# Optimization experiments

Measured on AMD Instinct MI355X. Metric: run time of the kernel, lower is better.

Reference implementation:

```python
import jax, jax.numpy as jnp
import numpy as np

B, L, ENC_IN, DM, H, HD, DFF, NL, C_OUT = 4, 1024, 64, 512, 8, 64, 2048, 3, 64
SCALE = 1.0 / np.sqrt(HD)


def _ln(x, g, b):
    m = x.mean(-1, keepdims=True)
    v = ((x - m) ** 2).mean(-1, keepdims=True)
    return (x - m) / jnp.sqrt(v + 1e-5) * g + b


def _pos_encoding(length, d):
    pos = np.arange(length)[:, None].astype(np.float32)
    div = np.exp(np.arange(0, d, 2).astype(np.float32) * (-np.log(10000.0) / d))
    pe = np.zeros((length, d), np.float32)
    pe[:, 0::2] = np.sin(pos * div)
    pe[:, 1::2] = np.cos(pos * div)
    return jnp.asarray(pe)

PE = _pos_encoding(L, DM)


def _prob_attn(q, k, v, idx):
    # q,k,v: [B,H,L,D]; idx: [L, sample_k] random key indices per query
    qk = jnp.einsum('bhqd,bhkd->bhqk', q, k)                       # [B,H,L,L]
    qks = jnp.take_along_axis(qk, idx[None, None, :, :], axis=-1)   # sampled QK
    M = qks.max(-1) - qks.sum(-1) / L                                # sparsity measure [B,H,L]
    _, top = jax.lax.top_k(M, L)  # n_top == L here (degenerate full selection / permutation)
    scores = jnp.take_along_axis(qk, top[..., None], axis=2) * SCALE  # gathered Q rows
    A = jax.nn.softmax(scores, axis=-1)
    return jnp.einsum('bhuk,bhkd->bhud', A, v)                       # [B,H,L,D]


def _forward(x_enc, sample_idx, W_emb, b_emb, Wq, bq, Wk, bk, Wv, bv, Wo, bo,
             W1, b1, W2, b2, g1, be1, g2, be2, gN, bN, W_proj, b_proj):
    x = x_enc @ W_emb + b_emb + PE[None]  # [B,L,DM]
    for i in range(NL):
        q = (x @ Wq[i] + bq[i]).reshape(B, L, H, HD).transpose(0, 2, 1, 3)
        k = (x @ Wk[i] + bk[i]).reshape(B, L, H, HD).transpose(0, 2, 1, 3)
        v = (x @ Wv[i] + bv[i]).reshape(B, L, H, HD).transpose(0, 2, 1, 3)
        o = _prob_attn(q, k, v, sample_idx[i]).transpose(0, 2, 1, 3).reshape(B, L, DM)
        o = o @ Wo[i] + bo[i]
        x = _ln(x + o, g1[i], be1[i])
        y = jax.nn.gelu(x @ W1[i] + b1[i], approximate=False) @ W2[i] + b2[i]
        x = _ln(x + y, g2[i], be2[i])
    x = _ln(x, gN, bN)
    return x @ W_proj + b_proj


def setup_inputs() -> dict:
    key = jax.random.key(0)
    ks = jax.random.split(key, 16)
    nrm = lambda k, s: jax.random.normal(k, s, jnp.float32) * 0.02
    return {
        'x_enc': jax.random.normal(ks[0], (B, L, ENC_IN), jnp.float32),
        'sample_idx': jax.random.randint(ks[1], (NL, L, L), 0, L, dtype=jnp.int32),
        'W_emb': nrm(ks[2], (ENC_IN, DM)), 'b_emb': jnp.zeros((DM,), jnp.float32),
        'Wq': nrm(ks[3], (NL, DM, DM)), 'bq': jnp.zeros((NL, DM), jnp.float32),
        'Wk': nrm(ks[4], (NL, DM, DM)), 'bk': jnp.zeros((NL, DM), jnp.float32),
        'Wv': nrm(ks[5], (NL, DM, DM)), 'bv': jnp.zeros((NL, DM), jnp.float32),
        'Wo': nrm(ks[6], (NL, DM, DM)), 'bo': jnp.zeros((NL, DM), jnp.float32),
        'W1': nrm(ks[7], (NL, DM, DFF)), 'b1': jnp.zeros((NL, DFF), jnp.float32),
        'W2': nrm(ks[8], (NL, DFF, DM)), 'b2': jnp.zeros((NL, DM), jnp.float32),
        'g1': jnp.ones((NL, DM), jnp.float32), 'be1': jnp.zeros((NL, DM), jnp.float32),
        'g2': jnp.ones((NL, DM), jnp.float32), 'be2': jnp.zeros((NL, DM), jnp.float32),
        'gN': jnp.ones((DM,), jnp.float32), 'bN': jnp.zeros((DM,), jnp.float32),
        'W_proj': nrm(ks[9], (DM, C_OUT)), 'b_proj': jnp.zeros((C_OUT,), jnp.float32),
    }


def reference(x_enc, sample_idx, W_emb, b_emb, Wq, bq, Wk, bk, Wv, bv, Wo, bo,
              W1, b1, W2, b2, g1, be1, g2, be2, gN, bN, W_proj, b_proj):
    return _forward(x_enc, sample_idx, W_emb, b_emb, Wq, bq, Wk, bk, Wv, bv, Wo, bo,
                    W1, b1, W2, b2, g1, be1, g2, be2, gN, bN, W_proj, b_proj)
```

## Files before the change

### kernel.cpp

```cpp
#include <hip/hip_runtime.h>
#include <cstdint>
#include <cstddef>

#define B_    4
#define L_    1024
#define ENCIN 64
#define DM    512
#define H_    8
#define HD    64
#define DFF   2048
#define NL    3
#define COUT  64
#define SCALE 0.125f
#define BH    32

typedef __attribute__((ext_vector_type(4))) short short4v;
typedef __attribute__((ext_vector_type(8))) short short8v;
typedef __attribute__((ext_vector_type(4))) float f32x4;
typedef unsigned short u16;

#define MFMA16(a,b,c) __builtin_amdgcn_mfma_f32_16x16x32_bf16(a,b,c,0,0,0)

#define GL2LDS(gsrc, ldst) \
  __builtin_amdgcn_global_load_lds( \
      (const __attribute__((address_space(1))) void*)(uintptr_t)(const void*)(gsrc), \
      (__attribute__((address_space(3))) void*)(uintptr_t)(const void*)(ldst), 16, 0, 0)

__device__ __forceinline__ u16 f2bf(float f){
  unsigned u = __float_as_uint(f);
  u += 0x7fffu + ((u >> 16) & 1u);
  return (u16)(u >> 16);
}
__device__ __forceinline__ float bf2f(u16 h){
  return __uint_as_float(((unsigned)h) << 16);
}
__device__ __forceinline__ void split2(float v, u16* h, u16* l){
  u16 hh = f2bf(v);
  *h = hh;
  *l = f2bf(v - bf2f(hh));
}

template<int BN, int MODE>
__global__ __launch_bounds__(256) void hgemm(
    const u16* __restrict__ Ah, const u16* __restrict__ Al,
    const u16* __restrict__ Bh, const u16* __restrict__ Bl,
    const float* __restrict__ bias,
    float* __restrict__ o32, u16* __restrict__ oh, u16* __restrict__ ol,
    int M, int N, int K)
{
  constexpr int NT = BN / 32;
  __shared__ u16 As0[128*32], As1[128*32];
  __shared__ u16 Bs0[BN*32],  Bs1[BN*32];
  const int t = threadIdx.x, lane = t & 63, wid = t >> 6;
  const int wr = wid >> 1, wc = wid & 1;
  const int fr = lane & 15, fq = lane >> 4;
  const int m0 = blockIdx.y * 128, n0 = blockIdx.x * BN;
  const int arow = lane >> 2, aseg = lane & 3;

  f32x4 acc[4][NT] = {};

  for (int kt = 0; kt < K; kt += 32) {
#pragma unroll
    for (int i = 0; i < 2; i++) {
      int c = wid + 4*i;
      GL2LDS(&Ah[(size_t)(m0 + c*16 + arow)*K + kt + aseg*8], &As0[c*512]);
      GL2LDS(&Al[(size_t)(m0 + c*16 + arow)*K + kt + aseg*8], &As1[c*512]);
    }
#pragma unroll
    for (int i = 0; i < BN/64; i++) {
      int c = wid + 4*i;
      GL2LDS(&Bh[(size_t)(n0 + c*16 + arow)*K + kt + aseg*8], &Bs0[c*512]);
      GL2LDS(&Bl[(size_t)(n0 + c*16 + arow)*K + kt + aseg*8], &Bs1[c*512]);
    }
    __syncthreads();

    short8v a0[4], a1[4], b0[NT], b1[NT];
#pragma unroll
    for (int m = 0; m < 4; m++) {
      int off = (wr*64 + m*16 + fr)*32 + fq*4;
      short4v x0 = *(const short4v*)&As0[off];
      short4v x1 = *(const short4v*)&As0[off + 16];
      a0[m] = __builtin_shufflevector(x0, x1, 0,1,2,3,4,5,6,7);
      short4v y0 = *(const short4v*)&As1[off];
      short4v y1 = *(const short4v*)&As1[off + 16];
      a1[m] = __builtin_shufflevector(y0, y1, 0,1,2,3,4,5,6,7);
    }
#pragma unroll
    for (int n = 0; n < NT; n++) {
      int off = (wc*(BN/2) + n*16 + fr)*32 + fq*4;
      short4v x0 = *(const short4v*)&Bs0[off];
      short4v x1 = *(const short4v*)&Bs0[off + 16];
      b0[n] = __builtin_shufflevector(x0, x1, 0,1,2,3,4,5,6,7);
      short4v y0 = *(const short4v*)&Bs1[off];
      short4v y1 = *(const short4v*)&Bs1[off + 16];
      b1[n] = __builtin_shufflevector(y0, y1, 0,1,2,3,4,5,6,7);
    }
#pragma unroll
    for (int m = 0; m < 4; m++)
#pragma unroll
      for (int n = 0; n < NT; n++) {
        acc[m][n] = MFMA16(a0[m], b0[n], acc[m][n]);
        acc[m][n] = MFMA16(a0[m], b1[n], acc[m][n]);
        acc[m][n] = MFMA16(a1[m], b0[n], acc[m][n]);
      }
    __syncthreads();
  }

#pragma unroll
  for (int m = 0; m < 4; m++) {
    int gr0 = m0 + wr*64 + m*16 + fq*4;
#pragma unroll
    for (int n = 0; n < NT; n++) {
      int gc = n0 + wc*(BN/2) + n*16 + fr;
      float bv = bias[gc];
#pragma unroll
      for (int r = 0; r < 4; r++) {
        float v = acc[m][n][r] + bv;
        int row = gr0 + r;
        if (MODE == 0) {
          o32[(size_t)row*N + gc] = v;
        } else if (MODE == 1) {
          int li = row & (L_ - 1);
          float dv = expf((float)(gc & ~1) * -0.017988946039015984f);
          float ang = (float)li * dv;
          v += (gc & 1) ? cosf(ang) : sinf(ang);
          size_t ix = (size_t)row*N + gc;
          o32[ix] = v;
          split2(v, &oh[ix], &ol[ix]);
        } else if (MODE == 2) {
          float gv = 0.5f * v * (1.0f + erff(v * 0.70710678118654752f));
          size_t ix = (size_t)row*N + gc;
          split2(gv, &oh[ix], &ol[ix]);
        } else if (MODE == 3) {
          int b = row >> 10, li = row & (L_ - 1);
          int hh2 = gc >> 6, d = gc & 63;
          size_t ix = (((size_t)(b*H_ + hh2))*L_ + li)*HD + d;
          split2(v, &oh[ix], &ol[ix]);
        } else if (MODE == 4) {
          int b = row >> 10, li = row & (L_ - 1);
          int hh2 = gc >> 6, d = gc & 63;
          size_t ix = (((size_t)(b*H_ + hh2))*HD + d)*L_ + li;
          oh[ix] = f2bf(v);
        }
      }
    }
  }
}

__global__ __launch_bounds__(256) void qk_mfma(
    const u16* __restrict__ qh, const u16* __restrict__ ql,
    const u16* __restrict__ kh, const u16* __restrict__ kl,
    float* __restrict__ S)
{
  __shared__ u16 Qs0[128*64], Qs1[128*64], Ks0[128*64], Ks1[128*64];
  const int t = threadIdx.x, lane = t & 63, wid = t >> 6;
  const int wr = wid >> 1, wc = wid & 1;
  const int fr = lane & 15, fq = lane >> 4;
  const int n0 = blockIdx.x * 128, m0 = blockIdx.y * 128, bh = blockIdx.z;
  const int arow = lane >> 3, aseg = lane & 7;
  const u16* qhb = qh + (size_t)bh * L_ * HD;
  const u16* qlb = ql + (size_t)bh * L_ * HD;
  const u16* khb = kh + (size_t)bh * L_ * HD;
  const u16* klb = kl + (size_t)bh * L_ * HD;

#pragma unroll
  for (int i = 0; i < 4; i++) {
    int c = wid + 4*i;
    GL2LDS(&qhb[(size_t)(m0 + c*8 + arow)*HD + aseg*8], &Qs0[c*512]);
    GL2LDS(&qlb[(size_t)(m0 + c*8 + arow)*HD + aseg*8], &Qs1[c*512]);
    GL2LDS(&khb[(size_t)(n0 + c*8 + arow)*HD + aseg*8], &Ks0[c*512]);
    GL2LDS(&klb[(size_t)(n0 + c*8 + arow)*HD + aseg*8], &Ks1[c*512]);
  }
  __syncthreads();

  f32x4 acc[4][4] = {};
#pragma unroll
  for (int ks = 0; ks < 2; ks++) {
    int kg = ks*32 + fq*4;
    short8v a0[4], a1[4], b0[4], b1[4];
#pragma unroll
    for (int m = 0; m < 4; m++) {
      int off = (wr*64 + m*16 + fr)*64 + kg;
      short4v x0 = *(const short4v*)&Qs0[off];
      short4v x1 = *(const short4v*)&Qs0[off + 16];
      a0[m] = __builtin_shufflevector(x0, x1, 0,1,2,3,4,5,6,7);
      short4v y0 = *(const short4v*)&Qs1[off];
      short4v y1 = *(const short4v*)&Qs1[off + 16];
      a1[m] = __builtin_shufflevector(y0, y1, 0,1,2,3,4,5,6,7);
    }
#pragma unroll
    for (int n = 0; n < 4; n++) {
      int off = (wc*64 + n*16 + fr)*64 + kg;
      short4v x0 = *(const short4v*)&Ks0[off];
      short4v x1 = *(const short4v*)&Ks0[off + 16];
      b0[n] = __builtin_shufflevector(x0, x1, 0,1,2,3,4,5,6,7);
      short4v y0 = *(const short4v*)&Ks1[off];
      short4v y1 = *(const short4v*)&Ks1[off + 16];
      b1[n] = __builtin_shufflevector(y0, y1, 0,1,2,3,4,5,6,7);
    }
#pragma unroll
    for (int m = 0; m < 4; m++)
#pragma unroll
      for (int n = 0; n < 4; n++) {
        acc[m][n] = MFMA16(a0[m], b0[n], acc[m][n]);
        acc[m][n] = MFMA16(a0[m], b1[n], acc[m][n]);
        acc[m][n] = MFMA16(a1[m], b0[n], acc[m][n]);
      }
  }

#pragma unroll
  for (int m = 0; m < 4; m++)
#pragma unroll
    for (int n = 0; n < 4; n++)
#pragma unroll
      for (int r = 0; r < 4; r++) {
        int grow = m0 + wr*64 + m*16 + fq*4 + r;
        int gcol = n0 + wc*64 + n*16 + fr;
        S[((size_t)bh*L_ + grow)*L_ + gcol] = acc[m][n][r];
      }
}

__global__ __launch_bounds__(256) void m_k(const float* __restrict__ S,
    const int* __restrict__ idx, float* __restrict__ Mv)
{
  const int qi = blockIdx.x, bh = blockIdx.y, t = threadIdx.x;
  const float* row = S + ((size_t)bh * L_ + qi) * L_;
  const int* ir = idx + (size_t)qi * L_;
  float mx = -1e30f, sm = 0.f;
  for (int s = t; s < L_; s += 256) {
    float v = row[ir[s]];
    mx = fmaxf(mx, v);
    sm += v;
  }
#pragma unroll
  for (int o = 32; o > 0; o >>= 1) {
    mx = fmaxf(mx, __shfl_xor(mx, o));
    sm += __shfl_xor(sm, o);
  }
  __shared__ float wmx[4], wsm[4];
  if ((t & 63) == 0) { wmx[t >> 6] = mx; wsm[t >> 6] = sm; }
  __syncthreads();
  if (t == 0) {
    mx = fmaxf(fmaxf(wmx[0], wmx[1]), fmaxf(wmx[2], wmx[3]));
    sm = wsm[0] + wsm[1] + wsm[2] + wsm[3];
    Mv[(size_t)bh * L_ + qi] = mx - sm * (1.0f / L_);
  }
}

__global__ __launch_bounds__(256) void sm_k(const float* __restrict__ S,
    float* __restrict__ rmax, float* __restrict__ rsum)
{
  const int row = blockIdx.x, bh = blockIdx.y, t = threadIdx.x;
  const float4* rf = (const float4*)&S[((size_t)bh*L_ + row)*L_];
  float4 v = rf[t];
  float mx = fmaxf(fmaxf(v.x, v.y), fmaxf(v.z, v.w));
  __shared__ float red[4], red2[4];
#pragma unroll
  for (int o = 32; o > 0; o >>= 1) mx = fmaxf(mx, __shfl_xor(mx, o));
  if ((t & 63) == 0) red[t >> 6] = mx;
  __syncthreads();
  mx = fmaxf(fmaxf(red[0], red[1]), fmaxf(red[2], red[3])) * SCALE;
  float sm = expf(v.x*SCALE - mx) + expf(v.y*SCALE - mx) +
             expf(v.z*SCALE - mx) + expf(v.w*SCALE - mx);
#pragma unroll
  for (int o = 32; o > 0; o >>= 1) sm += __shfl_xor(sm, o);
  if ((t & 63) == 0) red2[t >> 6] = sm;
  __syncthreads();
  if (t == 0) {
    rmax[(size_t)bh*L_ + row] = mx;
    rsum[(size_t)bh*L_ + row] = red2[0] + red2[1] + red2[2] + red2[3];
  }
}

__global__ __launch_bounds__(1024) void sort_k(const float* __restrict__ Mv,
                                               int* __restrict__ rank)
{
  __shared__ unsigned long long keys[L_];
  const int bh = blockIdx.x, t = threadIdx.x;
  float m = Mv[(size_t)bh * L_ + t];
  unsigned u = __float_as_uint(m);
  u = (u & 0x80000000u) ? ~u : (u | 0x80000000u);
  keys[t] = ((unsigned long long)(~u) << 32) | (unsigned)t;
  __syncthreads();
  for (int k = 2; k <= L_; k <<= 1) {
    for (int j = k >> 1; j > 0; j >>= 1) {
      int ixj = t ^ j;
      if (ixj > t) {
        unsigned long long a = keys[t], b = keys[ixj];
        bool up = ((t & k) == 0);
        if ((a > b) == up) { keys[t] = b; keys[ixj] = a; }
      }
      __syncthreads();
    }
  }
  int orig = (int)(keys[t] & 0xFFFFFFFFu);
  rank[(size_t)bh * L_ + orig] = t;
}

__global__ __launch_bounds__(256) void pv_mfma(
    const float* __restrict__ S, const u16* __restrict__ vt,
    const float* __restrict__ rmx, const float* __restrict__ rsm,
    const int* __restrict__ rank,
    u16* __restrict__ ath, u16* __restrict__ atl)
{
  __shared__ u16 Ps[128*64];
  __shared__ u16 Vs[64*64];
  __shared__ float rmaxS[128], rsumS[128];
  __shared__ int rankS[128];
  const int t = threadIdx.x, lane = t & 63, wid = t >> 6;
  const int wr = wid >> 1, wc = wid & 1;
  const int fr = lane & 15, fq = lane >> 4;
  const int l0 = blockIdx.x * 128, bh = blockIdx.y;
  const int bb = bh >> 3, hh = bh & 7;
  const int arow = lane >> 3, aseg = lane & 7;

  if (t < 128) {
    rmaxS[t] = rmx[(size_t)bh*L_ + l0 + t];
    rsumS[t] = rsm[(size_t)bh*L_ + l0 + t];
    rankS[t] = rank[(size_t)bh*L_ + l0 + t];
  }
  __syncthreads();

  f32x4 acc[4][2] = {};
  for (int c0 = 0; c0 < L_; c0 += 64) {
#pragma unroll
    for (int i = 0; i < 2; i++) {
      int c = wid + 4*i;
      GL2LDS(&vt[((size_t)bh*HD + c*8 + arow)*L_ + c0 + aseg*8], &Vs[c*512]);
    }
#pragma unroll
    for (int i = 0; i < 8; i++) {
      int f = t + 256*i;
      int row = f >> 4, q = f & 15;
      float4 s4 = *(const float4*)&S[((size_t)bh*L_ + l0 + row)*L_ + c0 + q*4];
      float mxr = rmaxS[row];
      short4v p4 = { (short)f2bf(expf(s4.x*SCALE - mxr)),
                     (short)f2bf(expf(s4.y*SCALE - mxr)),
                     (short)f2bf(expf(s4.z*SCALE - mxr)),
                     (short)f2bf(expf(s4.w*SCALE - mxr)) };
      *(short4v*)&Ps[row*64 + q*4] = p4;
    }
    __syncthreads();
#pragma unroll
    for (int ks = 0; ks < 2; ks++) {
      int kg = ks*32 + fq*4;
      short8v a[4], b[2];
#pragma unroll
      for (int m = 0; m < 4; m++) {
        int off = (wr*64 + m*16 + fr)*64 + kg;
        short4v x0 = *(const short4v*)&Ps[off];
        short4v x1 = *(const short4v*)&Ps[off + 16];
        a[m] = __builtin_shufflevector(x0, x1, 0,1,2,3,4,5,6,7);
      }
#pragma unroll
      for (int n = 0; n < 2; n++) {
        int off = (wc*32 + n*16 + fr)*64 + kg;
        short4v x0 = *(const short4v*)&Vs[off];
        short4v x1 = *(const short4v*)&Vs[off + 16];
        b[n] = __builtin_shufflevector(x0, x1, 0,1,2,3,4,5,6,7);
      }
#pragma unroll
      for (int m = 0; m < 4; m++)
#pragma unroll
        for (int n = 0; n < 2; n++)
          acc[m][n] = MFMA16(a[m], b[n], acc[m][n]);
    }
    __syncthreads();
  }

#pragma unroll
  for (int m = 0; m < 4; m++)
#pragma unroll
    for (int n = 0; n < 2; n++)
#pragma unroll
      for (int r = 0; r < 4; r++) {
        int lrow = wr*64 + m*16 + fq*4 + r;
        int u = rankS[lrow];
        int d = wc*32 + n*16 + fr;
        float o = acc[m][n][r] / rsumS[lrow];
        size_t ix = ((size_t)bb*L_ + u)*DM + hh*HD + d;
        split2(o, &ath[ix], &atl[ix]);
      }
}

__global__ __launch_bounds__(64) void ln_k(const float* __restrict__ xin,
    const float* __restrict__ add, const float* __restrict__ g,
    const float* __restrict__ bb, float* __restrict__ out,
    u16* __restrict__ oh, u16* __restrict__ ol)
{
  const int row = blockIdx.x, t = threadIdx.x;
  const float4* xf = (const float4*)(xin + (size_t)row * DM);
  float4 v0 = xf[t], v1 = xf[t + 64];
  if (add) {
    const float4* af = (const float4*)(add + (size_t)row * DM);
    float4 a0 = af[t], a1 = af[t + 64];
    v0.x += a0.x; v0.y += a0.y; v0.z += a0.z; v0.w += a0.w;
    v1.x += a1.x; v1.y += a1.y; v1.z += a1.z; v1.w += a1.w;
  }
  float s  = v0.x + v0.y + v0.z + v0.w + v1.x + v1.y + v1.z + v1.w;
  float ss = v0.x*v0.x + v0.y*v0.y + v0.z*v0.z + v0.w*v0.w +
             v1.x*v1.x + v1.y*v1.y + v1.z*v1.z + v1.w*v1.w;
#pragma unroll
  for (int o = 32; o > 0; o >>= 1) { s += __shfl_xor(s, o); ss += __shfl_xor(ss, o); }
  float mean = s * (1.0f / DM);
  float var  = ss * (1.0f / DM) - mean * mean;
  float inv  = 1.0f / sqrtf(var + 1e-5f);
  const float4* gf = (const float4*)g;
  const float4* bf = (const float4*)bb;
  float4 g0 = gf[t], g1 = gf[t + 64], b0 = bf[t], b1 = bf[t + 64];
  float o0[4], o1[4];
  o0[0] = (v0.x-mean)*inv*g0.x + b0.x; o0[1] = (v0.y-mean)*inv*g0.y + b0.y;
  o0[2] = (v0.z-mean)*inv*g0.z + b0.z; o0[3] = (v0.w-mean)*inv*g0.w + b0.w;
  o1[0] = (v1.x-mean)*inv*g1.x + b1.x; o1[1] = (v1.y-mean)*inv*g1.y + b1.y;
  o1[2] = (v1.z-mean)*inv*g1.z + b1.z; o1[3] = (v1.w-mean)*inv*g1.w + b1.w;
  float4* of = (float4*)(out + (size_t)row * DM);
  of[t]      = make_float4(o0[0], o0[1], o0[2], o0[3]);
  of[t + 64] = make_float4(o1[0], o1[1], o1[2], o1[3]);
  size_t base = (size_t)row * DM;
#pragma unroll
  for (int j = 0; j < 4; j++) {
    split2(o0[j], &oh[base + t*4 + j],       &ol[base + t*4 + j]);
    split2(o1[j], &oh[base + 256 + t*4 + j], &ol[base + 256 + t*4 + j]);
  }
}

__global__ __launch_bounds__(256) void wt_k(const float* __restrict__ W,
    u16* __restrict__ Th, u16* __restrict__ Tl, int K, int N)
{
  __shared__ float tile[32][33];
  const int k0 = blockIdx.y * 32, n0 = blockIdx.x * 32;
  const int c = threadIdx.x & 31, r4 = threadIdx.x >> 5;
#pragma unroll
  for (int i = 0; i < 4; i++) {
    int r = r4 * 4 + i;
    tile[r][c] = W[(size_t)(k0 + r) * N + n0 + c];
  }
  __syncthreads();
#pragma unroll
  for (int i = 0; i < 4; i++) {
    int r = r4 * 4 + i;
    float v = tile[c][r];
    split2(v, &Th[(size_t)(n0 + r) * K + k0 + c], &Tl[(size_t)(n0 + r) * K + k0 + c]);
  }
}

__global__ __launch_bounds__(256) void split_k(const float* __restrict__ in,
    u16* __restrict__ oh, u16* __restrict__ ol, int n4)
{
  int i = blockIdx.x * 256 + threadIdx.x;
  if (i < n4) {
    float4 v = ((const float4*)in)[i];
    split2(v.x, &oh[i*4+0], &ol[i*4+0]);
    split2(v.y, &oh[i*4+1], &ol[i*4+1]);
    split2(v.z, &oh[i*4+2], &ol[i*4+2]);
    split2(v.w, &oh[i*4+3], &ol[i*4+3]);
  }
}

extern "C" void kernel_launch(void* const* d_in, const int* in_sizes, int n_in,
                              void* d_out, int out_size, void* d_ws, size_t ws_size,
                              hipStream_t stream)
{
  const float* x_enc   = (const float*)d_in[0];
  const int*   sidx    = (const int*)d_in[1];
  const float* W_emb   = (const float*)d_in[2];
  const float* b_emb   = (const float*)d_in[3];
  const float* Wq      = (const float*)d_in[4];
  const float* bq      = (const float*)d_in[5];
  const float* Wk      = (const float*)d_in[6];
  const float* bk      = (const float*)d_in[7];
  const float* Wv      = (const float*)d_in[8];
  const float* bv      = (const float*)d_in[9];
  const float* Wo      = (const float*)d_in[10];
  const float* bo      = (const float*)d_in[11];
  const float* W1      = (const float*)d_in[12];
  const float* b1      = (const float*)d_in[13];
  const float* W2      = (const float*)d_in[14];
  const float* b2      = (const float*)d_in[15];
  const float* g1      = (const float*)d_in[16];
  const float* be1     = (const float*)d_in[17];
  const float* g2      = (const float*)d_in[18];
  const float* be2     = (const float*)d_in[19];
  const float* gN      = (const float*)d_in[20];
  const float* bN      = (const float*)d_in[21];
  const float* W_proj  = (const float*)d_in[22];
  const float* b_proj  = (const float*)d_in[23];

  const int M = B_ * L_;
  char* w = (char*)d_ws;
  float* S   = (float*)w;  w += (size_t)BH * L_ * L_ * 4;
  float* x   = (float*)w;  w += (size_t)M * DM * 4;
  u16* xh    = (u16*)w;    w += (size_t)M * DM * 2;
  u16* xl    = (u16*)w;    w += (size_t)M * DM * 2;
  u16* qh_   = (u16*)w;    w += (size_t)BH * L_ * HD * 2;
  u16* ql_   = (u16*)w;    w += (size_t)BH * L_ * HD * 2;
  u16* kh_   = (u16*)w;    w += (size_t)BH * L_ * HD * 2;
  u16* kl_   = (u16*)w;    w += (size_t)BH * L_ * HD * 2;
  u16* vt_   = (u16*)w;    w += (size_t)BH * L_ * HD * 2;
  u16* ath   = (u16*)w;    w += (size_t)M * DM * 2;
  u16* atl   = (u16*)w;    w += (size_t)M * DM * 2;
  float* rmx_ = (float*)w; w += (size_t)BH * L_ * 4;
  float* rsm_ = (float*)w; w += (size_t)BH * L_ * 4;
  float* Mv_  = (float*)w; w += (size_t)BH * L_ * 4;
  int* rank_  = (int*)w;   w += (size_t)BH * L_ * 4;
  u16* WqTh = (u16*)w; w += (size_t)DM*DM*2;
  u16* WqTl = (u16*)w; w += (size_t)DM*DM*2;
  u16* WkTh = (u16*)w; w += (size_t)DM*DM*2;
  u16* WkTl = (u16*)w; w += (size_t)DM*DM*2;
  u16* WvTh = (u16*)w; w += (size_t)DM*DM*2;
  u16* WvTl = (u16*)w; w += (size_t)DM*DM*2;
  u16* WoTh = (u16*)w; w += (size_t)DM*DM*2;
  u16* WoTl = (u16*)w; w += (size_t)DM*DM*2;
  u16* W1Th = (u16*)w; w += (size_t)DFF*DM*2;
  u16* W1Tl = (u16*)w; w += (size_t)DFF*DM*2;
  u16* W2Th = (u16*)w; w += (size_t)DM*DFF*2;
  u16* W2Tl = (u16*)w; w += (size_t)DM*DFF*2;
  u16* WeTh = (u16*)w; w += (size_t)DM*ENCIN*2;
  u16* WeTl = (u16*)w; w += (size_t)DM*ENCIN*2;
  u16* WpTh = (u16*)w; w += (size_t)COUT*DM*2;
  u16* WpTl = (u16*)w; w += (size_t)COUT*DM*2;
  u16* yh  = (u16*)S;
  u16* yl  = (u16*)((char*)S + (size_t)M*DFF*2);
  float* tmp = (float*)((char*)S + 2*(size_t)M*DFF*2);
  u16* xeh = (u16*)((char*)S + 64u*1024u*1024u);
  u16* xel = xeh + (size_t)M*ENCIN;

  split_k<<<dim3((M*ENCIN/4 + 255)/256), 256, 0, stream>>>(x_enc, xeh, xel, M*ENCIN/4);
  wt_k<<<dim3(DM/32, ENCIN/32), 256, 0, stream>>>(W_emb, WeTh, WeTl, ENCIN, DM);
  wt_k<<<dim3(COUT/32, DM/32), 256, 0, stream>>>(W_proj, WpTh, WpTl, DM, COUT);
  hgemm<64,1><<<dim3(DM/64, M/128), 256, 0, stream>>>(
      xeh, xel, WeTh, WeTl, b_emb, x, xh, xl, M, DM, ENCIN);

  for (int il = 0; il < NL; il++) {
    wt_k<<<dim3(DM/32, DM/32), 256, 0, stream>>>(Wq + (size_t)il*DM*DM, WqTh, WqTl, DM, DM);
    wt_k<<<dim3(DM/32, DM/32), 256, 0, stream>>>(Wk + (size_t)il*DM*DM, WkTh, WkTl, DM, DM);
    wt_k<<<dim3(DM/32, DM/32), 256, 0, stream>>>(Wv + (size_t)il*DM*DM, WvTh, WvTl, DM, DM);
    wt_k<<<dim3(DM/32, DM/32), 256, 0, stream>>>(Wo + (size_t)il*DM*DM, WoTh, WoTl, DM, DM);
    wt_k<<<dim3(DFF/32, DM/32), 256, 0, stream>>>(W1 + (size_t)il*DM*DFF, W1Th, W1Tl, DM, DFF);
    wt_k<<<dim3(DM/32, DFF/32), 256, 0, stream>>>(W2 + (size_t)il*DFF*DM, W2Th, W2Tl, DFF, DM);

    hgemm<64,3><<<dim3(DM/64, M/128), 256, 0, stream>>>(
        xh, xl, WqTh, WqTl, bq + il*DM, nullptr, qh_, ql_, M, DM, DM);
    hgemm<64,3><<<dim3(DM/64, M/128), 256, 0, stream>>>(
        xh, xl, WkTh, WkTl, bk + il*DM, nullptr, kh_, kl_, M, DM, DM);
    hgemm<64,4><<<dim3(DM/64, M/128), 256, 0, stream>>>(
        xh, xl, WvTh, WvTl, bv + il*DM, nullptr, vt_, nullptr, M, DM, DM);

    qk_mfma<<<dim3(L_/128, L_/128, BH), 256, 0, stream>>>(qh_, ql_, kh_, kl_, S);
    m_k<<<dim3(L_, BH), 256, 0, stream>>>(S, sidx + (size_t)il*L_*L_, Mv_);
    sm_k<<<dim3(L_, BH), 256, 0, stream>>>(S, rmx_, rsm_);
    sort_k<<<BH, 1024, 0, stream>>>(Mv_, rank_);
    pv_mfma<<<dim3(L_/128, BH), 256, 0, stream>>>(S, vt_, rmx_, rsm_, rank_, ath, atl);

    hgemm<64,0><<<dim3(DM/64, M/128), 256, 0, stream>>>(
        ath, atl, WoTh, WoTl, bo + il*DM, tmp, nullptr, nullptr, M, DM, DM);
    ln_k<<<M, 64, 0, stream>>>(x, tmp, g1 + il*DM, be1 + il*DM, x, xh, xl);

    hgemm<128,2><<<dim3(DFF/128, M/128), 256, 0, stream>>>(
        xh, xl, W1Th, W1Tl, b1 + il*DFF, nullptr, yh, yl, M, DFF, DM);
    hgemm<64,0><<<dim3(DM/64, M/128), 256, 0, stream>>>(
        yh, yl, W2Th, W2Tl, b2 + il*DM, tmp, nullptr, nullptr, M, DM, DFF);
    ln_k<<<M, 64, 0, stream>>>(x, tmp, g2 + il*DM, be2 + il*DM, x, xh, xl);
  }

  ln_k<<<M, 64, 0, stream>>>(x, nullptr, gN, bN, x, xh, xl);
  hgemm<64,0><<<dim3(COUT/64, M/128), 256, 0, stream>>>(
      xh, xl, WpTh, WpTl, b_proj, (float*)d_out, nullptr, nullptr, M, COUT, DM);
}
```

Before: 2.075 ms.

## Fuse QKV GEMM, double-buffer hgemm, split-K Wo/W2, fuse softmax stats into QK

```diff
diff --git a/kernel.cpp b/kernel.cpp
--- a/kernel.cpp
+++ b/kernel.cpp
@@ -40,65 +40,75 @@
   *l = f2bf(v - bf2f(hh));
 }
 
-template<int BN, int MODE>
+template<int MODE>
 __global__ __launch_bounds__(256) void hgemm(
     const u16* __restrict__ Ah, const u16* __restrict__ Al,
     const u16* __restrict__ Bh, const u16* __restrict__ Bl,
-    const float* __restrict__ bias,
+    const float* __restrict__ bias1, const float* __restrict__ bias2,
+    const float* __restrict__ bias3,
     float* __restrict__ o32, u16* __restrict__ oh, u16* __restrict__ ol,
-    int M, int N, int K)
-{
-  constexpr int NT = BN / 32;
-  __shared__ u16 As0[128*32], As1[128*32];
-  __shared__ u16 Bs0[BN*32],  Bs1[BN*32];
+    u16* __restrict__ oh2, u16* __restrict__ ol2, u16* __restrict__ ov,
+    int Mtot, int N, int K, int klen)
+{
+  __shared__ u16 As[2][2][128*32];
+  __shared__ u16 Bs[2][2][64*32];
   const int t = threadIdx.x, lane = t & 63, wid = t >> 6;
   const int wr = wid >> 1, wc = wid & 1;
   const int fr = lane & 15, fq = lane >> 4;
-  const int m0 = blockIdx.y * 128, n0 = blockIdx.x * BN;
-  const int arow = lane >> 2, aseg = lane & 3;
-
-  f32x4 acc[4][NT] = {};
-
-  for (int kt = 0; kt < K; kt += 32) {
+  const int m0 = blockIdx.y * 128, n0 = blockIdx.x * 64;
+  const int z = blockIdx.z;
+  const int kbase = z * klen;
+  const int srow = lane >> 2, sseg = lane & 3;
+
+  const int nk = klen / 32;
+
+  auto stage = [&](int buf, int kt) {
 #pragma unroll
     for (int i = 0; i < 2; i++) {
       int c = wid + 4*i;
-      GL2LDS(&Ah[(size_t)(m0 + c*16 + arow)*K + kt + aseg*8], &As0[c*512]);
-      GL2LDS(&Al[(size_t)(m0 + c*16 + arow)*K + kt + aseg*8], &As1[c*512]);
-    }
-#pragma unroll
-    for (int i = 0; i < BN/64; i++) {
-      int c = wid + 4*i;
-      GL2LDS(&Bh[(size_t)(n0 + c*16 + arow)*K + kt + aseg*8], &Bs0[c*512]);
-      GL2LDS(&Bl[(size_t)(n0 + c*16 + arow)*K + kt + aseg*8], &Bs1[c*512]);
-    }
-    __syncthreads();
-
-    short8v a0[4], a1[4], b0[NT], b1[NT];
+      GL2LDS(&Ah[(size_t)(m0 + c*16 + srow)*K + kt + sseg*8], &As[buf][0][c*512]);
+      GL2LDS(&Al[(size_t)(m0 + c*16 + srow)*K + kt + sseg*8], &As[buf][1][c*512]);
+    }
+    {
+      int c = wid;
+      GL2LDS(&Bh[(size_t)(n0 + c*16 + srow)*K + kt + sseg*8], &Bs[buf][0][c*512]);
+      GL2LDS(&Bl[(size_t)(n0 + c*16 + srow)*K + kt + sseg*8], &Bs[buf][1][c*512]);
+    }
+  };
+
+  f32x4 acc[4][2] = {};
+  stage(0, kbase);
+  __syncthreads();
+
+  for (int it = 0; it < nk; ++it) {
+    int cur = it & 1;
+    if (it + 1 < nk) stage(cur ^ 1, kbase + (it+1)*32);
+
+    short8v a0[4], a1[4], b0[2], b1[2];
 #pragma unroll
     for (int m = 0; m < 4; m++) {
       int off = (wr*64 + m*16 + fr)*32 + fq*4;
-      short4v x0 = *(const short4v*)&As0[off];
-      short4v x1 = *(const short4v*)&As0[off + 16];
+      short4v x0 = *(const short4v*)&As[cur][0][off];
+      short4v x1 = *(const short4v*)&As[cur][0][off + 16];
       a0[m] = __builtin_shufflevector(x0, x1, 0,1,2,3,4,5,6,7);
-      short4v y0 = *(const short4v*)&As1[off];
-      short4v y1 = *(const short4v*)&As1[off + 16];
+      short4v y0 = *(const short4v*)&As[cur][1][off];
+      short4v y1 = *(const short4v*)&As[cur][1][off + 16];
       a1[m] = __builtin_shufflevector(y0, y1, 0,1,2,3,4,5,6,7);
     }
 #pragma unroll
-    for (int n = 0; n < NT; n++) {
-      int off = (wc*(BN/2) + n*16 + fr)*32 + fq*4;
-      short4v x0 = *(const short4v*)&Bs0[off];
-      short4v x1 = *(const short4v*)&Bs0[off + 16];
+    for (int n = 0; n < 2; n++) {
+      int off = (wc*32 + n*16 + fr)*32 + fq*4;
+      short4v x0 = *(const short4v*)&Bs[cur][0][off];
+      short4v x1 = *(const short4v*)&Bs[cur][0][off + 16];
       b0[n] = __builtin_shufflevector(x0, x1, 0,1,2,3,4,5,6,7);
-      short4v y0 = *(const short4v*)&Bs1[off];
-      short4v y1 = *(const short4v*)&Bs1[off + 16];
+      short4v y0 = *(const short4v*)&Bs[cur][1][off];
+      short4v y1 = *(const short4v*)&Bs[cur][1][off + 16];
       b1[n] = __builtin_shufflevector(y0, y1, 0,1,2,3,4,5,6,7);
     }
 #pragma unroll
     for (int m = 0; m < 4; m++)
 #pragma unroll
-      for (int n = 0; n < NT; n++) {
+      for (int n = 0; n < 2; n++) {
         acc[m][n] = MFMA16(a0[m], b0[n], acc[m][n]);
         acc[m][n] = MFMA16(a0[m], b1[n], acc[m][n]);
         acc[m][n] = MFMA16(a1[m], b0[n], acc[m][n]);
@@ -108,18 +118,19 @@
 
 #pragma unroll
   for (int m = 0; m < 4; m++) {
-    int gr0 = m0 + wr*64 + m*16 + fq*4;
-#pragma unroll
-    for (int n = 0; n < NT; n++) {
-      int gc = n0 + wc*(BN/2) + n*16 + fr;
-      float bv = bias[gc];
+#pragma unroll
+    for (int n = 0; n < 2; n++) {
+      int gc = n0 + wc*32 + n*16 + fr;
 #pragma unroll
       for (int r = 0; r < 4; r++) {
-        float v = acc[m][n][r] + bv;
-        int row = gr0 + r;
-        if (MODE == 0) {
-          o32[(size_t)row*N + gc] = v;
+        int row = m0 + wr*64 + m*16 + fq*4 + r;
+        float v = acc[m][n][r];
+        if (MODE == 5) {
+          o32[((size_t)z*Mtot + row)*N + gc] = v;
+        } else if (MODE == 0) {
+          o32[(size_t)row*N + gc] = v + bias1[gc];
         } else if (MODE == 1) {
+          v += bias1[gc];
           int li = row & (L_ - 1);
           float dv = expf((float)(gc & ~1) * -0.017988946039015984f);
           float ang = (float)li * dv;
@@ -128,19 +139,26 @@
           o32[ix] = v;
           split2(v, &oh[ix], &ol[ix]);
         } else if (MODE == 2) {
+          v += bias1[gc];
           float gv = 0.5f * v * (1.0f + erff(v * 0.70710678118654752f));
           size_t ix = (size_t)row*N + gc;
           split2(gv, &oh[ix], &ol[ix]);
         } else if (MODE == 3) {
           int b = row >> 10, li = row & (L_ - 1);
-          int hh2 = gc >> 6, d = gc & 63;
-          size_t ix = (((size_t)(b*H_ + hh2))*L_ + li)*HD + d;
-          split2(v, &oh[ix], &ol[ix]);
-        } else if (MODE == 4) {
-          int b = row >> 10, li = row & (L_ - 1);
-          int hh2 = gc >> 6, d = gc & 63;
-          size_t ix = (((size_t)(b*H_ + hh2))*HD + d)*L_ + li;
-          oh[ix] = f2bf(v);
+          int sub = gc >> 9, h = (gc >> 6) & 7, d = gc & 63;
+          if (sub == 0) {
+            v += bias1[gc];
+            size_t ix = (((size_t)(b*H_ + h))*L_ + li)*HD + d;
+            split2(v, &oh[ix], &ol[ix]);
+          } else if (sub == 1) {
+            v += bias2[gc - 512];
+            size_t ix = (((size_t)(b*H_ + h))*L_ + li)*HD + d;
+            split2(v, &oh2[ix], &ol2[ix]);
+          } else {
+            v += bias3[gc - 1024];
+            size_t ix = (((size_t)(b*H_ + h))*HD + d)*L_ + li;
+            ov[ix] = f2bf(v);
+          }
         }
       }
     }
@@ -150,14 +168,14 @@
 __global__ __launch_bounds__(256) void qk_mfma(
     const u16* __restrict__ qh, const u16* __restrict__ ql,
     const u16* __restrict__ kh, const u16* __restrict__ kl,
-    float* __restrict__ S)
+    float* __restrict__ S, float* __restrict__ pmax, float* __restrict__ psum)
 {
   __shared__ u16 Qs0[128*64], Qs1[128*64], Ks0[128*64], Ks1[128*64];
   const int t = threadIdx.x, lane = t & 63, wid = t >> 6;
   const int wr = wid >> 1, wc = wid & 1;
   const int fr = lane & 15, fq = lane >> 4;
   const int n0 = blockIdx.x * 128, m0 = blockIdx.y * 128, bh = blockIdx.z;
-  const int arow = lane >> 3, aseg = lane & 7;
+  const int srow = lane >> 3, sseg = lane & 7;
   const u16* qhb = qh + (size_t)bh * L_ * HD;
   const u16* qlb = ql + (size_t)bh * L_ * HD;
   const u16* khb = kh + (size_t)bh * L_ * HD;
@@ -166,10 +184,10 @@
 #pragma unroll
   for (int i = 0; i < 4; i++) {
     int c = wid + 4*i;
-    GL2LDS(&qhb[(size_t)(m0 + c*8 + arow)*HD + aseg*8], &Qs0[c*512]);
-    GL2LDS(&qlb[(size_t)(m0 + c*8 + arow)*HD + aseg*8], &Qs1[c*512]);
-    GL2LDS(&khb[(size_t)(n0 + c*8 + arow)*HD + aseg*8], &Ks0[c*512]);
-    GL2LDS(&klb[(size_t)(n0 + c*8 + arow)*HD + aseg*8], &Ks1[c*512]);
+    GL2LDS(&qhb[(size_t)(m0 + c*8 + srow)*HD + sseg*8], &Qs0[c*512]);
+    GL2LDS(&qlb[(size_t)(m0 + c*8 + srow)*HD + sseg*8], &Qs1[c*512]);
+    GL2LDS(&khb[(size_t)(n0 + c*8 + srow)*HD + sseg*8], &Ks0[c*512]);
+    GL2LDS(&klb[(size_t)(n0 + c*8 + srow)*HD + sseg*8], &Ks1[c*512]);
   }
   __syncthreads();
 
@@ -218,6 +236,50 @@
         int gcol = n0 + wc*64 + n*16 + fr;
         S[((size_t)bh*L_ + grow)*L_ + gcol] = acc[m][n][r];
       }
+
+  const int tix = blockIdx.x*2 + wc;
+#pragma unroll
+  for (int m = 0; m < 4; m++) {
+    float mx[4], sm[4];
+#pragma unroll
+    for (int r = 0; r < 4; r++) {
+      float v = fmaxf(fmaxf(acc[m][0][r], acc[m][1][r]),
+                      fmaxf(acc[m][2][r], acc[m][3][r]));
+#pragma unroll
+      for (int o2 = 1; o2 < 16; o2 <<= 1) v = fmaxf(v, __shfl_xor(v, o2));
+      mx[r] = v * SCALE;
+      float s = 0.f;
+#pragma unroll
+      for (int n = 0; n < 4; n++) s += expf(acc[m][n][r]*SCALE - mx[r]);
+#pragma unroll
+      for (int o2 = 1; o2 < 16; o2 <<= 1) s += __shfl_xor(s, o2);
+      sm[r] = s;
+    }
+    if (fr == 0) {
+#pragma unroll
+      for (int r = 0; r < 4; r++) {
+        int grow = m0 + wr*64 + m*16 + fq*4 + r;
+        size_t ix = ((size_t)bh*L_ + grow)*16 + tix;
+        pmax[ix] = mx[r];
+        psum[ix] = sm[r];
+      }
+    }
+  }
+}
+
+__global__ __launch_bounds__(256) void smc_k(const float* __restrict__ pmax,
+    const float* __restrict__ psum, float* __restrict__ rmx, float* __restrict__ rsm)
+{
+  const int g = threadIdx.x & 15;
+  const size_t flat = (size_t)blockIdx.x*16 + (threadIdx.x >> 4);
+  float m = pmax[flat*16 + g], s = psum[flat*16 + g];
+  float gm = m;
+#pragma unroll
+  for (int o = 1; o < 16; o <<= 1) gm = fmaxf(gm, __shfl_xor(gm, o));
+  float gs = s * expf(m - gm);
+#pragma unroll
+  for (int o = 1; o < 16; o <<= 1) gs += __shfl_xor(gs, o);
+  if (g == 0) { rmx[flat] = gm; rsm[flat] = gs; }
 }
 
 __global__ __launch_bounds__(256) void m_k(const float* __restrict__ S,
@@ -244,31 +306,6 @@
     mx = fmaxf(fmaxf(wmx[0], wmx[1]), fmaxf(wmx[2], wmx[3]));
     sm = wsm[0] + wsm[1] + wsm[2] + wsm[3];
     Mv[(size_t)bh * L_ + qi] = mx - sm * (1.0f / L_);
-  }
-}
-
-__global__ __launch_bounds__(256) void sm_k(const float* __restrict__ S,
-    float* __restrict__ rmax, float* __restrict__ rsum)
-{
-  const int row = blockIdx.x, bh = blockIdx.y, t = threadIdx.x;
-  const float4* rf = (const float4*)&S[((size_t)bh*L_ + row)*L_];
-  float4 v = rf[t];
-  float mx = fmaxf(fmaxf(v.x, v.y), fmaxf(v.z, v.w));
-  __shared__ float red[4], red2[4];
-#pragma unroll
-  for (int o = 32; o > 0; o >>= 1) mx = fmaxf(mx, __shfl_xor(mx, o));
-  if ((t & 63) == 0) red[t >> 6] = mx;
-  __syncthreads();
-  mx = fmaxf(fmaxf(red[0], red[1]), fmaxf(red[2], red[3])) * SCALE;
-  float sm = expf(v.x*SCALE - mx) + expf(v.y*SCALE - mx) +
-             expf(v.z*SCALE - mx) + expf(v.w*SCALE - mx);
-#pragma unroll
-  for (int o = 32; o > 0; o >>= 1) sm += __shfl_xor(sm, o);
-  if ((t & 63) == 0) red2[t >> 6] = sm;
-  __syncthreads();
-  if (t == 0) {
-    rmax[(size_t)bh*L_ + row] = mx;
-    rsum[(size_t)bh*L_ + row] = red2[0] + red2[1] + red2[2] + red2[3];
   }
 }
 
@@ -303,33 +340,33 @@
     const int* __restrict__ rank,
     u16* __restrict__ ath, u16* __restrict__ atl)
 {
-  __shared__ u16 Ps[128*64];
+  __shared__ u16 Ps[64*64];
   __shared__ u16 Vs[64*64];
-  __shared__ float rmaxS[128], rsumS[128];
-  __shared__ int rankS[128];
+  __shared__ float rmaxS[64], rsumS[64];
+  __shared__ int rankS[64];
   const int t = threadIdx.x, lane = t & 63, wid = t >> 6;
   const int wr = wid >> 1, wc = wid & 1;
   const int fr = lane & 15, fq = lane >> 4;
-  const int l0 = blockIdx.x * 128, bh = blockIdx.y;
+  const int l0 = blockIdx.x * 64, bh = blockIdx.y;
   const int bb = bh >> 3, hh = bh & 7;
-  const int arow = lane >> 3, aseg = lane & 7;
-
-  if (t < 128) {
+  const int srow = lane >> 3, sseg = lane & 7;
+
+  if (t < 64) {
     rmaxS[t] = rmx[(size_t)bh*L_ + l0 + t];
     rsumS[t] = rsm[(size_t)bh*L_ + l0 + t];
     rankS[t] = rank[(size_t)bh*L_ + l0 + t];
   }
   __syncthreads();
 
-  f32x4 acc[4][2] = {};
+  f32x4 acc[2][2] = {};
   for (int c0 = 0; c0 < L_; c0 += 64) {
 #pragma unroll
     for (int i = 0; i < 2; i++) {
       int c = wid + 4*i;
-      GL2LDS(&vt[((size_t)bh*HD + c*8 + arow)*L_ + c0 + aseg*8], &Vs[c*512]);
-    }
-#pragma unroll
-    for (int i = 0; i < 8; i++) {
+      GL2LDS(&vt[((size_t)bh*HD + c*8 + srow)*L_ + c0 + sseg*8], &Vs[c*512]);
+    }
+#pragma unroll
+    for (int i = 0; i < 4; i++) {
       int f = t + 256*i;
       int row = f >> 4, q = f & 15;
       float4 s4 = *(const float4*)&S[((size_t)bh*L_ + l0 + row)*L_ + c0 + q*4];
@@ -344,10 +381,10 @@
 #pragma unroll
     for (int ks = 0; ks < 2; ks++) {
       int kg = ks*32 + fq*4;
-      short8v a[4], b[2];
-#pragma unroll
-      for (int m = 0; m < 4; m++) {
-        int off = (wr*64 + m*16 + fr)*64 + kg;
+      short8v a[2], b[2];
+#pragma unroll
+      for (int m = 0; m < 2; m++) {
+        int off = (wr*32 + m*16 + fr)*64 + kg;
         short4v x0 = *(const short4v*)&Ps[off];
         short4v x1 = *(const short4v*)&Ps[off + 16];
         a[m] = __builtin_shufflevector(x0, x1, 0,1,2,3,4,5,6,7);
@@ -360,7 +397,7 @@
         b[n] = __builtin_shufflevector(x0, x1, 0,1,2,3,4,5,6,7);
       }
 #pragma unroll
-      for (int m = 0; m < 4; m++)
+      for (int m = 0; m < 2; m++)
 #pragma unroll
         for (int n = 0; n < 2; n++)
           acc[m][n] = MFMA16(a[m], b[n], acc[m][n]);
@@ -369,12 +406,12 @@
   }
 
 #pragma unroll
-  for (int m = 0; m < 4; m++)
+  for (int m = 0; m < 2; m++)
 #pragma unroll
     for (int n = 0; n < 2; n++)
 #pragma unroll
       for (int r = 0; r < 4; r++) {
-        int lrow = wr*64 + m*16 + fq*4 + r;
+        int lrow = wr*32 + m*16 + fq*4 + r;
         int u = rankS[lrow];
         int d = wc*32 + n*16 + fr;
         float o = acc[m][n][r] / rsumS[lrow];
@@ -383,19 +420,25 @@
       }
 }
 
-__global__ __launch_bounds__(64) void ln_k(const float* __restrict__ xin,
-    const float* __restrict__ add, const float* __restrict__ g,
-    const float* __restrict__ bb, float* __restrict__ out,
-    u16* __restrict__ oh, u16* __restrict__ ol)
+__global__ __launch_bounds__(64) void ln2_k(const float* __restrict__ xin,
+    const float* __restrict__ part, int np, const float* __restrict__ bias,
+    const float* __restrict__ g, const float* __restrict__ bb,
+    float* __restrict__ out, u16* __restrict__ oh, u16* __restrict__ ol)
 {
   const int row = blockIdx.x, t = threadIdx.x;
   const float4* xf = (const float4*)(xin + (size_t)row * DM);
   float4 v0 = xf[t], v1 = xf[t + 64];
-  if (add) {
-    const float4* af = (const float4*)(add + (size_t)row * DM);
+  for (int p = 0; p < np; p++) {
+    const float4* af = (const float4*)(part + ((size_t)p*(B_*L_) + row) * DM);
     float4 a0 = af[t], a1 = af[t + 64];
     v0.x += a0.x; v0.y += a0.y; v0.z += a0.z; v0.w += a0.w;
     v1.x += a1.x; v1.y += a1.y; v1.z += a1.z; v1.w += a1.w;
+  }
+  if (bias) {
+    const float4* cf = (const float4*)bias;
+    float4 c0 = cf[t], c1 = cf[t + 64];
+    v0.x += c0.x; v0.y += c0.y; v0.z += c0.z; v0.w += c0.w;
+    v1.x += c1.x; v1.y += c1.y; v1.z += c1.z; v1.w += c1.w;
   }
   float s  = v0.x + v0.y + v0.z + v0.w + v1.x + v1.y + v1.z + v1.w;
   float ss = v0.x*v0.x + v0.y*v0.y + v0.z*v0.z + v0.w*v0.w +
@@ -425,8 +468,12 @@
 }
 
 __global__ __launch_bounds__(256) void wt_k(const float* __restrict__ W,
-    u16* __restrict__ Th, u16* __restrict__ Tl, int K, int N)
-{
+    u16* __restrict__ Th, u16* __restrict__ Tl, int K, int N,
+    size_t wz, size_t tz)
+{
+  W  += (size_t)blockIdx.z * wz;
+  Th += (size_t)blockIdx.z * tz;
+  Tl += (size_t)blockIdx.z * tz;
   __shared__ float tile[32][33];
   const int k0 = blockIdx.y * 32, n0 = blockIdx.x * 32;
   const int c = threadIdx.x & 31, r4 = threadIdx.x >> 5;
@@ -503,67 +550,72 @@
   float* rsm_ = (float*)w; w += (size_t)BH * L_ * 4;
   float* Mv_  = (float*)w; w += (size_t)BH * L_ * 4;
   int* rank_  = (int*)w;   w += (size_t)BH * L_ * 4;
-  u16* WqTh = (u16*)w; w += (size_t)DM*DM*2;
-  u16* WqTl = (u16*)w; w += (size_t)DM*DM*2;
-  u16* WkTh = (u16*)w; w += (size_t)DM*DM*2;
-  u16* WkTl = (u16*)w; w += (size_t)DM*DM*2;
-  u16* WvTh = (u16*)w; w += (size_t)DM*DM*2;
-  u16* WvTl = (u16*)w; w += (size_t)DM*DM*2;
-  u16* WoTh = (u16*)w; w += (size_t)DM*DM*2;
-  u16* WoTl = (u16*)w; w += (size_t)DM*DM*2;
-  u16* W1Th = (u16*)w; w += (size_t)DFF*DM*2;
-  u16* W1Tl = (u16*)w; w += (size_t)DFF*DM*2;
-  u16* W2Th = (u16*)w; w += (size_t)DM*DFF*2;
-  u16* W2Tl = (u16*)w; w += (size_t)DM*DFF*2;
-  u16* WeTh = (u16*)w; w += (size_t)DM*ENCIN*2;
-  u16* WeTl = (u16*)w; w += (size_t)DM*ENCIN*2;
-  u16* WpTh = (u16*)w; w += (size_t)COUT*DM*2;
-  u16* WpTl = (u16*)w; w += (size_t)COUT*DM*2;
-  u16* yh  = (u16*)S;
-  u16* yl  = (u16*)((char*)S + (size_t)M*DFF*2);
-  float* tmp = (float*)((char*)S + 2*(size_t)M*DFF*2);
-  u16* xeh = (u16*)((char*)S + 64u*1024u*1024u);
-  u16* xel = xeh + (size_t)M*ENCIN;
+  float* pmax_ = (float*)w; w += (size_t)BH * L_ * 16 * 4;
+  float* psum_ = (float*)w; w += (size_t)BH * L_ * 16 * 4;
+  u16* WqkvTh = (u16*)w; w += (size_t)NL*1536*DM*2;
+  u16* WqkvTl = (u16*)w; w += (size_t)NL*1536*DM*2;
+  u16* WoTh   = (u16*)w; w += (size_t)NL*DM*DM*2;
+  u16* WoTl   = (u16*)w; w += (size_t)NL*DM*DM*2;
+  u16* W1Th   = (u16*)w; w += (size_t)NL*DFF*DM*2;
+  u16* W1Tl   = (u16*)w; w += (size_t)NL*DFF*DM*2;
+  u16* W2Th   = (u16*)w; w += (size_t)NL*DM*DFF*2;
+  u16* W2Tl   = (u16*)w; w += (size_t)NL*DM*DFF*2;
+  u16* WeTh   = (u16*)w; w += (size_t)DM*ENCIN*2;
+  u16* WeTl   = (u16*)w; w += (size_t)DM*ENCIN*2;
+  u16* WpTh   = (u16*)w; w += (size_t)COUT*DM*2;
+  u16* WpTl   = (u16*)w; w += (size_t)COUT*DM*2;
+  u16*   yh     = (u16*)S;
+  u16*   yl     = (u16*)((char*)S + 16u*1024u*1024u);
+  float* partWo = (float*)((char*)S + 32u*1024u*1024u);
+  float* partW2 = (float*)((char*)S + 48u*1024u*1024u);
+  u16*   xeh    = (u16*)((char*)S + 80u*1024u*1024u);
+  u16*   xel    = xeh + (size_t)M*ENCIN;
 
   split_k<<<dim3((M*ENCIN/4 + 255)/256), 256, 0, stream>>>(x_enc, xeh, xel, M*ENCIN/4);
-  wt_k<<<dim3(DM/32, ENCIN/32), 256, 0, stream>>>(W_emb, WeTh, WeTl, ENCIN, DM);
-  wt_k<<<dim3(COUT/32, DM/32), 256, 0, stream>>>(W_proj, WpTh, WpTl, DM, COUT);
-  hgemm<64,1><<<dim3(DM/64, M/128), 256, 0, stream>>>(
-      xeh, xel, WeTh, WeTl, b_emb, x, xh, xl, M, DM, ENCIN);
+  wt_k<<<dim3(DM/32, DM/32, NL), 256, 0, stream>>>(Wq, WqkvTh,            WqkvTl,            DM, DM, (size_t)DM*DM, (size_t)1536*DM);
+  wt_k<<<dim3(DM/32, DM/32, NL), 256, 0, stream>>>(Wk, WqkvTh + 512*DM,   WqkvTl + 512*DM,   DM, DM, (size_t)DM*DM, (size_t)1536*DM);
+  wt_k<<<dim3(DM/32, DM/32, NL), 256, 0, stream>>>(Wv, WqkvTh + 1024*DM,  WqkvTl + 1024*DM,  DM, DM, (size_t)DM*DM, (size_t)1536*DM);
+  wt_k<<<dim3(DM/32, DM/32, NL), 256, 0, stream>>>(Wo, WoTh, WoTl, DM, DM, (size_t)DM*DM, (size_t)DM*DM);
+  wt_k<<<dim3(DFF/32, DM/32, NL), 256, 0, stream>>>(W1, W1Th, W1Tl, DM, DFF, (size_t)DM*DFF, (size_t)DFF*DM);
+  wt_k<<<dim3(DM/32, DFF/32, NL), 256, 0, stream>>>(W2, W2Th, W2Tl, DFF, DM, (size_t)DFF*DM, (size_t)DM*DFF);
+  wt_k<<<dim3(DM/32, ENCIN/32, 1), 256, 0, stream>>>(W_emb, WeTh, WeTl, ENCIN, DM, 0, 0);
+  wt_k<<<dim3(COUT/32, DM/32, 1), 256, 0, stream>>>(W_proj, WpTh, WpTl, DM, COUT, 0, 0);
+
+  hgemm<1><<<dim3(DM/64, M/128, 1), 256, 0, stream>>>(
+      xeh, xel, WeTh, WeTl, b_emb, nullptr, nullptr,
+      x, xh, xl, nullptr, nullptr, nullptr, M, DM, ENCIN, ENCIN);
 
   for (int il = 0; il < NL; il++) {
-    wt_k<<<dim3(DM/32, DM/32), 256, 0, stream>>>(Wq + (size_t)il*DM*DM, WqTh, WqTl, DM, DM);
-    wt_k<<<dim3(DM/32, DM/32), 256, 0, stream>>>(Wk + (size_t)il*DM*DM, WkTh, WkTl, DM, DM);
-    wt_k<<<dim3(DM/32, DM/32), 256, 0, stream>>>(Wv + (size_t)il*DM*DM, WvTh, WvTl, DM, DM);
-    wt_k<<<dim3(DM/32, DM/32), 256, 0, stream>>>(Wo + (size_t)il*DM*DM, WoTh, WoTl, DM, DM);
-    wt_k<<<dim3(DFF/32, DM/32), 256, 0, stream>>>(W1 + (size_t)il*DM*DFF, W1Th, W1Tl, DM, DFF);
-    wt_k<<<dim3(DM/32, DFF/32), 256, 0, stream>>>(W2 + (size_t)il*DFF*DM, W2Th, W2Tl, DFF, DM);
-
-    hgemm<64,3><<<dim3(DM/64, M/128), 256, 0, stream>>>(
-        xh, xl, WqTh, WqTl, bq + il*DM, nullptr, qh_, ql_, M, DM, DM);
-    hgemm<64,3><<<dim3(DM/64, M/128), 256, 0, stream>>>(
-        xh, xl, WkTh, WkTl, bk + il*DM, nullptr, kh_, kl_, M, DM, DM);
-    hgemm<64,4><<<dim3(DM/64, M/128), 256, 0, stream>>>(
-        xh, xl, WvTh, WvTl, bv + il*DM, nullptr, vt_, nullptr, M, DM, DM);
-
-    qk_mfma<<<dim3(L_/128, L_/128, BH), 256, 0, stream>>>(qh_, ql_, kh_, kl_, S);
+    hgemm<3><<<dim3(1536/64, M/128, 1), 256, 0, stream>>>(
+        xh, xl, WqkvTh + (size_t)il*1536*DM, WqkvTl + (size_t)il*1536*DM,
+        bq + il*DM, bk + il*DM, bv + il*DM,
+        nullptr, qh_, ql_, kh_, kl_, vt_, M, 1536, DM, DM);
+
+    qk_mfma<<<dim3(L_/128, L_/128, BH), 256, 0, stream>>>(qh_, ql_, kh_, kl_, S, pmax_, psum_);
+    smc_k<<<dim3(BH*L_/16), 256, 0, stream>>>(pmax_, psum_, rmx_, rsm_);
     m_k<<<dim3(L_, BH), 256, 0, stream>>>(S, sidx + (size_t)il*L_*L_, Mv_);
-    sm_k<<<dim3(L_, BH), 256, 0, stream>>>(S, rmx_, rsm_);
     sort_k<<<BH, 1024, 0, stream>>>(Mv_, rank_);
-    pv_mfma<<<dim3(L_/128, BH), 256, 0, stream>>>(S, vt_, rmx_, rsm_, rank_, ath, atl);
-
-    hgemm<64,0><<<dim3(DM/64, M/128), 256, 0, stream>>>(
-        ath, atl, WoTh, WoTl, bo + il*DM, tmp, nullptr, nullptr, M, DM, DM);
-    ln_k<<<M, 64, 0, stream>>>(x, tmp, g1 + il*DM, be1 + il*DM, x, xh, xl);
-
-    hgemm<128,2><<<dim3(DFF/128, M/128), 256, 0, stream>>>(
-        xh, xl, W1Th, W1Tl, b1 + il*DFF, nullptr, yh, yl, M, DFF, DM);
-    hgemm<64,0><<<dim3(DM/64, M/128), 256, 0, stream>>>(
-        yh, yl, W2Th, W2Tl, b2 + il*DM, tmp, nullptr, nullptr, M, DM, DFF);
-    ln_k<<<M, 64, 0, stream>>>(x, tmp, g2 + il*DM, be2 + il*DM, x, xh, xl);
-  }
-
-  ln_k<<<M, 64, 0, stream>>>(x, nullptr, gN, bN, x, xh, xl);
-  hgemm<64,0><<<dim3(COUT/64, M/128), 256, 0, stream>>>(
-      xh, xl, WpTh, WpTl, b_proj, (float*)d_out, nullptr, nullptr, M, COUT, DM);
-}
+    pv_mfma<<<dim3(L_/64, BH), 256, 0, stream>>>(S, vt_, rmx_, rsm_, rank_, ath, atl);
+
+    hgemm<5><<<dim3(DM/64, M/128, 2), 256, 0, stream>>>(
+        ath, atl, WoTh + (size_t)il*DM*DM, WoTl + (size_t)il*DM*DM,
+        nullptr, nullptr, nullptr,
+        partWo, nullptr, nullptr, nullptr, nullptr, nullptr, M, DM, DM, DM/2);
+    ln2_k<<<M, 64, 0, stream>>>(x, partWo, 2, bo + il*DM, g1 + il*DM, be1 + il*DM, x, xh, xl);
+
+    hgemm<2><<<dim3(DFF/64, M/128, 1), 256, 0, stream>>>(
+        xh, xl, W1Th + (size_t)il*DFF*DM, W1Tl + (size_t)il*DFF*DM,
+        b1 + il*DFF, nullptr, nullptr,
+        nullptr, yh, yl, nullptr, nullptr, nullptr, M, DFF, DM, DM);
+    hgemm<5><<<dim3(DM/64, M/128, 4), 256, 0, stream>>>(
+        yh, yl, W2Th + (size_t)il*DM*DFF, W2Tl + (size_t)il*DM*DFF,
+        nullptr, nullptr, nullptr,
+        partW2, nullptr, nullptr, nullptr, nullptr, nullptr, M, DM, DFF, DFF/4);
+    ln2_k<<<M, 64, 0, stream>>>(x, partW2, 4, b2 + il*DM, g2 + il*DM, be2 + il*DM, x, xh, xl);
+  }
+
+  ln2_k<<<M, 64, 0, stream>>>(x, nullptr, 0, nullptr, gN, bN, x, xh, xl);
+  hgemm<0><<<dim3(COUT/64, M/128, 1), 256, 0, stream>>>(
+      xh, xl, WpTh, WpTl, b_proj, nullptr, nullptr,
+      (float*)d_out, nullptr, nullptr, nullptr, nullptr, nullptr, M, COUT, DM, DM);
+}
```

Measured after the change: 1.803 ms. -13.1%, faster.
